# Kernel tuning notes

Measured on AMD Instinct MI355X. Metric: run time of the kernel, lower is better.

## Reference

```python
import jax, jax.numpy as jnp
import numpy as np

B, T, D = 16, 512, 256
HS, D_A, R = 512, 64, 8


def setup_inputs() -> dict:
    key = jax.random.key(0)
    ks = jax.random.split(key, 8)
    s = lambda *sh: 1.0 / np.sqrt(sh[0])
    x = jax.random.normal(ks[0], (B, T, D), dtype=jnp.float32)
    w_first = jax.random.normal(ks[1], (D, D_A), dtype=jnp.float32) * s(D)
    b_first = jnp.zeros((D_A,), dtype=jnp.float32)
    w_second = jax.random.normal(ks[2], (D_A, R), dtype=jnp.float32) * s(D_A)
    b_second = jnp.zeros((R,), dtype=jnp.float32)
    weight_iBarh = jax.random.normal(ks[3], (D, 4 * HS), dtype=jnp.float32) * s(D)
    weight_hh = jax.random.normal(ks[4], (HS, 4 * HS), dtype=jnp.float32) * s(HS)
    bias = jnp.zeros((4 * HS,), dtype=jnp.float32)
    return {"x": x, "w_first": w_first, "b_first": b_first,
            "w_second": w_second, "b_second": b_second,
            "weight_iBarh": weight_iBarh, "weight_hh": weight_hh, "bias": bias}


def _forward(x, w_first, b_first, w_second, b_second, weight_iBarh, weight_hh, bias):
    b, t, d = x.shape
    hs = weight_hh.shape[0]
    r = w_second.shape[1]
    # attention logits for every timestep: (B, T, r)
    s = jnp.tanh(x @ w_first + b_first) @ w_second + b_second
    # causal mask: query t attends to keys j <= t
    mask = jnp.tril(jnp.ones((t, t), dtype=bool))  # (t_query, j_key)
    # logits: (B, Tq, Tk, r); softmax over key axis per (t, r), masked to prefix
    logits = jnp.where(mask[None, :, :, None], s[:, None, :, :], -jnp.inf)
    attn = jax.nn.softmax(logits, axis=2).mean(axis=-1)  # (B, Tq, Tk) == mean over r
    # M_t = attention-weighted average of prefix inputs: (B, T, D)
    M = jnp.einsum('btj,bjd->btd', attn, x)
    gates_x = jnp.einsum('btd,dg->btg', M, weight_iBarh) + bias  # (B, T, 4H)

    def step(carry, gx):
        h, c = carry
        g = gx + h @ weight_hh  # (B, 4H)
        i = jax.nn.sigmoid(g[:, :hs])
        f = jax.nn.sigmoid(g[:, hs:2 * hs])
        gg = jnp.tanh(g[:, 2 * hs:3 * hs])
        o = jax.nn.sigmoid(g[:, 3 * hs:])
        c = f * c + i * gg
        h = o * jnp.tanh(c)
        return (h, c), h

    h0 = jnp.zeros((b, hs), dtype=x.dtype)
    c0 = jnp.zeros((b, hs), dtype=x.dtype)
    (h_t, c_t), hseq = jax.lax.scan(step, (h0, c0), jnp.swapaxes(gates_x, 0, 1))
    hidden_seq = jnp.swapaxes(hseq, 0, 1)  # (B, T, H)
    return hidden_seq, h_t, c_t


def reference(x, w_first, b_first, w_second, b_second, weight_iBarh, weight_hh, bias):
    return _forward(x, w_first, b_first, w_second, b_second, weight_iBarh, weight_hh, bias)
```

## Files before the change

### kernel.cpp

```cpp
#include <hip/hip_runtime.h>
#include <math.h>

#define BB 16
#define TT 512
#define DD 256
#define HS 512
#define DA 64
#define RR 8
#define G4H 2048


__global__ __launch_bounds__(256) void k1_score(
    const float* __restrict__ x, const float* __restrict__ w1,
    const float* __restrict__ b1, const float* __restrict__ w2,
    const float* __restrict__ b2, float* __restrict__ s_out) {
  const int wave = threadIdx.x >> 6;
  const int lane = threadIdx.x & 63;
  for (int i = 0; i < 4; ++i) {
    const int bt = blockIdx.x * 16 + wave * 4 + i;
    const float* xr = x + bt * DD;
    float acc = b1[lane];
    #pragma unroll 4
    for (int d = 0; d < DD; ++d)
      acc = fmaf(xr[d], w1[d * DA + lane], acc);
    const float a = tanhf(acc);
    #pragma unroll
    for (int r = 0; r < RR; ++r) {
      float v = a * w2[lane * RR + r];
      for (int off = 32; off > 0; off >>= 1) v += __shfl_xor(v, off);
      if (lane == 0) s_out[bt * RR + r] = v + b2[r];
    }
  }
}

__global__ __launch_bounds__(512) void k2_prefix(
    const float* __restrict__ s_in, float* __restrict__ e_out,
    float* __restrict__ inv_out) {
  const int b = blockIdx.x >> 3, r = blockIdx.x & 7;
  const int t = threadIdx.x;
  __shared__ float red[TT];
  __shared__ float buf[2][TT];
  const float v = s_in[(b * TT + t) * RR + r];
  red[t] = v;
  __syncthreads();
  for (int off = 256; off >= 1; off >>= 1) {
    if (t < off) red[t] = fmaxf(red[t], red[t + off]);
    __syncthreads();
  }
  const float m = red[0];
  const float e = expf(v - m);
  int p = 0;
  buf[0][t] = e;
  __syncthreads();
  for (int off = 1; off < TT; off <<= 1) {
    const float add = (t >= off) ? buf[p][t - off] : 0.f;
    buf[1 - p][t] = buf[p][t] + add;
    __syncthreads();
    p ^= 1;
  }
  const float den = buf[p][t];
  e_out[(b * TT + t) * RR + r] = e;
  inv_out[(b * TT + t) * RR + r] = 1.0f / den;
}

__global__ __launch_bounds__(64) void k3_mix(
    const float* __restrict__ x, const float* __restrict__ e_in,
    const float* __restrict__ inv_in, float* __restrict__ Mout) {
  const int b = blockIdx.x >> 2;
  const int d = (blockIdx.x & 3) * 64 + threadIdx.x;
  __shared__ __align__(16) float el[TT * RR];
  __shared__ __align__(16) float il[TT * RR];
  for (int i = threadIdx.x * 4; i < TT * RR; i += 64 * 4) {
    *(float4*)&el[i] = *(const float4*)&e_in[b * TT * RR + i];
    *(float4*)&il[i] = *(const float4*)&inv_in[b * TT * RR + i];
  }
  __syncthreads();
  float4 c0 = {0.f, 0.f, 0.f, 0.f}, c1 = {0.f, 0.f, 0.f, 0.f};
  for (int t = 0; t < TT; ++t) {
    const float xv = x[(b * TT + t) * DD + d];
    const float4 e0 = *(const float4*)&el[t * RR];
    const float4 e1 = *(const float4*)&el[t * RR + 4];
    const float4 i0 = *(const float4*)&il[t * RR];
    const float4 i1 = *(const float4*)&il[t * RR + 4];
    c0.x = fmaf(e0.x, xv, c0.x); c0.y = fmaf(e0.y, xv, c0.y);
    c0.z = fmaf(e0.z, xv, c0.z); c0.w = fmaf(e0.w, xv, c0.w);
    c1.x = fmaf(e1.x, xv, c1.x); c1.y = fmaf(e1.y, xv, c1.y);
    c1.z = fmaf(e1.z, xv, c1.z); c1.w = fmaf(e1.w, xv, c1.w);
    float msum = c0.x * i0.x + c0.y * i0.y + c0.z * i0.z + c0.w * i0.w;
    msum += c1.x * i1.x + c1.y * i1.y + c1.z * i1.z + c1.w * i1.w;
    Mout[(b * TT + t) * DD + d] = msum * 0.125f;
  }
}

__global__ __launch_bounds__(256) void k4_gemm(
    const float* __restrict__ A, const float* __restrict__ Bw,
    const float* __restrict__ bias, float* __restrict__ C) {
  const int bn = blockIdx.x & 15;
  const int bm = blockIdx.x >> 4;
  const int tid = threadIdx.x;
  const int tx = tid & 15, ty = tid >> 4;
  __shared__ __align__(16) float As[16][132];
  __shared__ __align__(16) float Bs[16][132];
  const int row0 = bm * 128, col0 = bn * 128;

  float acc[2][4][2][4];
  #pragma unroll
  for (int a = 0; a < 2; ++a)
    #pragma unroll
    for (int i = 0; i < 4; ++i)
      #pragma unroll
      for (int q = 0; q < 2; ++q)
        #pragma unroll
        for (int j = 0; j < 4; ++j) acc[a][i][q][j] = 0.f;

  const int arow = tid >> 1, akc = (tid & 1) * 8;
  const int bkr = tid >> 4, bcc = (tid & 15) * 8;

  for (int k0 = 0; k0 < 256; k0 += 16) {
    const float4 a0 = *(const float4*)&A[(row0 + arow) * 256 + k0 + akc];
    const float4 a1 = *(const float4*)&A[(row0 + arow) * 256 + k0 + akc + 4];
    const float4 b0 = *(const float4*)&Bw[(k0 + bkr) * 2048 + col0 + bcc];
    const float4 b1 = *(const float4*)&Bw[(k0 + bkr) * 2048 + col0 + bcc + 4];
    __syncthreads();
    As[akc + 0][arow] = a0.x; As[akc + 1][arow] = a0.y;
    As[akc + 2][arow] = a0.z; As[akc + 3][arow] = a0.w;
    As[akc + 4][arow] = a1.x; As[akc + 5][arow] = a1.y;
    As[akc + 6][arow] = a1.z; As[akc + 7][arow] = a1.w;
    *(float4*)&Bs[bkr][bcc] = b0;
    *(float4*)&Bs[bkr][bcc + 4] = b1;
    __syncthreads();
    #pragma unroll
    for (int kk = 0; kk < 16; ++kk) {
      float av[8], bv[8];
      *(float4*)&av[0] = *(const float4*)&As[kk][ty * 4];
      *(float4*)&av[4] = *(const float4*)&As[kk][64 + ty * 4];
      *(float4*)&bv[0] = *(const float4*)&Bs[kk][tx * 4];
      *(float4*)&bv[4] = *(const float4*)&Bs[kk][64 + tx * 4];
      #pragma unroll
      for (int a = 0; a < 2; ++a)
        #pragma unroll
        for (int i = 0; i < 4; ++i)
          #pragma unroll
          for (int q = 0; q < 2; ++q)
            #pragma unroll
            for (int j = 0; j < 4; ++j)
              acc[a][i][q][j] = fmaf(av[a * 4 + i], bv[q * 4 + j], acc[a][i][q][j]);
    }
  }
  const float4 bias0 = *(const float4*)&bias[col0 + tx * 4];
  const float4 bias1 = *(const float4*)&bias[col0 + 64 + tx * 4];
  #pragma unroll
  for (int a = 0; a < 2; ++a)
    #pragma unroll
    for (int i = 0; i < 4; ++i) {
      const int row = row0 + a * 64 + ty * 4 + i;
      float4 v0, v1;
      v0.x = acc[a][i][0][0] + bias0.x; v0.y = acc[a][i][0][1] + bias0.y;
      v0.z = acc[a][i][0][2] + bias0.z; v0.w = acc[a][i][0][3] + bias0.w;
      v1.x = acc[a][i][1][0] + bias1.x; v1.y = acc[a][i][1][1] + bias1.y;
      v1.z = acc[a][i][1][2] + bias1.z; v1.w = acc[a][i][1][3] + bias1.w;
      *(float4*)&C[row * 2048 + col0 + tx * 4] = v0;
      *(float4*)&C[row * 2048 + col0 + 64 + tx * 4] = v1;
    }
}

#define FMA4(ACC, W4, HSC)                         \
  ACC.x = fmaf((W4).x, (HSC), ACC.x);              \
  ACC.y = fmaf((W4).y, (HSC), ACC.y);              \
  ACC.z = fmaf((W4).z, (HSC), ACC.z);              \
  ACC.w = fmaf((W4).w, (HSC), ACC.w);

__device__ __forceinline__ float fast_sigmoid(float x) {
  return __builtin_amdgcn_rcpf(1.f + __expf(-x));
}
__device__ __forceinline__ float fast_tanh(float x) {
  const float xc = fmaxf(x, -30.f);
  const float e = __expf(-2.f * xc);
  return (1.f - e) * __builtin_amdgcn_rcpf(1.f + e);
}

__global__ __launch_bounds__(512, 1) void k5_lstm(
    const float* __restrict__ gates, const float* __restrict__ whh,
    float* __restrict__ out, unsigned long long* hbuf) {
  const int s   = blockIdx.x & 15;
  const int b   = blockIdx.x >> 4;
  const int tid = threadIdx.x;
  const int kq  = tid & 15;
  const int cq  = tid >> 4;
  const int j0  = s * 32;
  const int unit = j0 + cq;

  __shared__ __align__(16) float Wl[256 * 128];
  __shared__ __align__(16) float hl[2][576];

  float4 wr[32];
  for (int rnd = 0; rnd < 2; ++rnd) {
    for (int i = tid * 4; i < 256 * 128; i += 512 * 4) {
      const int k = i >> 7, c = i & 127;
      *(float4*)&Wl[i] =
          *(const float4*)&whh[(rnd * 256 + k) * G4H + (c >> 5) * HS + j0 + (c & 31)];
    }
    __syncthreads();
    if ((kq >> 3) == rnd) {
      const int kb = (kq & 7) * 32;
      #pragma unroll
      for (int kk = 0; kk < 32; ++kk) {
        const int base = (kb + kk) * 128 + cq;
        wr[kk].x = *(volatile const float*)&Wl[base];
        wr[kk].y = *(volatile const float*)&Wl[base + 32];
        wr[kk].z = *(volatile const float*)&Wl[base + 64];
        wr[kk].w = *(volatile const float*)&Wl[base + 96];
      }
    }
    __syncthreads();
  }

  float c_reg = 0.f;

  for (int t = 0; t < TT; ++t) {
    float gi = 0.f, gf = 0.f, gg = 0.f, go = 0.f;
    if (kq == 0) {
      const float* gt = gates + ((long)b * TT + t) * G4H + unit;
      gi = gt[0]; gf = gt[HS]; gg = gt[2 * HS]; go = gt[3 * HS];
    }
    const int par = t & 1;
    if (t > 0) {
      const unsigned long long* hsrc = hbuf + (((t - 1) & 1) * BB + b) * HS;
      unsigned long long pkt;
      do {
        pkt = __hip_atomic_load(&hsrc[tid], __ATOMIC_RELAXED,
                                __HIP_MEMORY_SCOPE_AGENT);
      } while ((unsigned)(pkt >> 32) < (unsigned)t);
      hl[par][(tid >> 5) * 36 + (tid & 31)] = __uint_as_float((unsigned)pkt);
    }
    __syncthreads();
    float4 acc = {0.f, 0.f, 0.f, 0.f};
    if (t > 0) {
      const float* hb = &hl[par][kq * 36];
      #pragma unroll
      for (int i = 0; i < 8; ++i) {
        const float4 h4 = *(const float4*)(hb + i * 4);
        FMA4(acc, wr[i * 4 + 0], h4.x);
        FMA4(acc, wr[i * 4 + 1], h4.y);
        FMA4(acc, wr[i * 4 + 2], h4.z);
        FMA4(acc, wr[i * 4 + 3], h4.w);
      }
    }
    #pragma unroll
    for (int off = 1; off <= 8; off <<= 1) {
      acc.x += __shfl_xor(acc.x, off); acc.y += __shfl_xor(acc.y, off);
      acc.z += __shfl_xor(acc.z, off); acc.w += __shfl_xor(acc.w, off);
    }
    if (kq == 0) {
      const float I = fast_sigmoid(acc.x + gi);
      const float F = fast_sigmoid(acc.y + gf);
      const float G = fast_tanh(acc.z + gg);
      const float O = fast_sigmoid(acc.w + go);
      c_reg = F * c_reg + I * G;
      const float h = O * fast_tanh(c_reg);
      const unsigned long long pkt =
          ((unsigned long long)(unsigned)(t + 1) << 32) |
          (unsigned long long)__float_as_uint(h);
      __hip_atomic_store(&hbuf[((t & 1) * BB + b) * HS + unit], pkt,
                         __ATOMIC_RELAXED, __HIP_MEMORY_SCOPE_AGENT);
      out[((long)b * TT + t) * HS + unit] = h;
      if (t == TT - 1) {
        out[(long)BB * TT * HS + b * HS + unit] = h;
        out[(long)BB * TT * HS + BB * HS + b * HS + unit] = c_reg;
      }
    }
  }
}

extern "C" void kernel_launch(void* const* d_in, const int* in_sizes, int n_in,
                              void* d_out, int out_size, void* d_ws,
                              size_t ws_size, hipStream_t stream) {
  const float* x    = (const float*)d_in[0];
  const float* w1   = (const float*)d_in[1];
  const float* b1   = (const float*)d_in[2];
  const float* w2   = (const float*)d_in[3];
  const float* b2   = (const float*)d_in[4];
  const float* wih  = (const float*)d_in[5];
  const float* whh  = (const float*)d_in[6];
  const float* bias = (const float*)d_in[7];
  float* out = (float*)d_out;

  float* ws = (float*)d_ws;
  float* s_buf  = ws;
  float* e_buf  = ws + 65536;
  float* i_buf  = ws + 131072;
  float* M_buf  = ws + 196608;
  float* g_buf  = ws + 2293760;
  unsigned long long* hbuf64 = (unsigned long long*)ws;

  k1_score<<<512, 256, 0, stream>>>(x, w1, b1, w2, b2, s_buf);
  k2_prefix<<<BB * RR, 512, 0, stream>>>(s_buf, e_buf, i_buf);
  k3_mix<<<64, 64, 0, stream>>>(x, e_buf, i_buf, M_buf);
  k4_gemm<<<64 * 16, 256, 0, stream>>>(M_buf, wih, bias, g_buf);
  hipMemsetAsync(hbuf64, 0, 2 * BB * HS * sizeof(unsigned long long), stream);
  k5_lstm<<<256, 512, 0, stream>>>(g_buf, whh, out, hbuf64);
}
```

Measured before the change: 1.141 ms.

## Use XCD-local sc0 polling for LSTM step handoff when batch group shares an XCD

Remaps block indices so the 16 slices of one batch element are likely placed on the same XCD, detects this at runtime via HW_REG_XCC_ID and a flag exchange, and then polls the hidden-state packets with sc0 loads that go through the XCD-local L2 instead of agent-scope atomics. Producers write with both an sc0 store and the agent-scope atomic store. If the fast poll stalls, it falls back to agent-scope polling. This is meant to cut per-timestep cross-block synchronization latency, at the cost of extra stores and reliance on undocumented cache-coherence behavior.

```diff
diff --git a/kernel.cpp b/kernel.cpp
--- a/kernel.cpp
+++ b/kernel.cpp
@@ -179,11 +179,27 @@
   return (1.f - e) * __builtin_amdgcn_rcpf(1.f + e);
 }
 
+#define HPOLL(Q) __hip_atomic_load((Q), __ATOMIC_RELAXED, __HIP_MEMORY_SCOPE_AGENT)
+
+__device__ __forceinline__ unsigned long long poll_sc0(
+    const unsigned long long* p) {
+  unsigned long long v;
+  asm volatile("global_load_dwordx2 %0, %1, off sc0\n\ts_waitcnt vmcnt(0)"
+               : "=v"(v) : "v"(p));
+  return v;
+}
+__device__ __forceinline__ void store_sc0(unsigned long long* p,
+                                          unsigned long long v) {
+  asm volatile("global_store_dwordx2 %0, %1, off sc0"
+               :: "v"(p), "v"(v) : "memory");
+}
+
 __global__ __launch_bounds__(512, 1) void k5_lstm(
     const float* __restrict__ gates, const float* __restrict__ whh,
-    float* __restrict__ out, unsigned long long* hbuf) {
-  const int s   = blockIdx.x & 15;
-  const int b   = blockIdx.x >> 4;
+    float* __restrict__ out, unsigned long long* hbuf,
+    unsigned long long* xflag) {
+  const int b   = blockIdx.x & 15;
+  const int s   = blockIdx.x >> 4;
   const int tid = threadIdx.x;
   const int kq  = tid & 15;
   const int cq  = tid >> 4;
@@ -192,6 +208,31 @@
 
   __shared__ __align__(16) float Wl[256 * 128];
   __shared__ __align__(16) float hl[2][576];
+  __shared__ int sflags[16];
+  __shared__ int s_same;
+
+  unsigned xcd;
+  asm volatile("s_getreg_b32 %0, hwreg(HW_REG_XCC_ID)" : "=s"(xcd));
+  if (tid == 0) {
+    const unsigned long long mypkt = (1ULL << 32) | (unsigned long long)xcd;
+    __hip_atomic_store(&xflag[b * 16 + s], mypkt, __ATOMIC_RELAXED,
+                       __HIP_MEMORY_SCOPE_AGENT);
+  }
+  if (tid < 16) {
+    unsigned long long v = 0; int sp = 0;
+    do {
+      v = HPOLL(&xflag[b * 16 + tid]);
+      if (++sp > 4096) break;
+    } while ((unsigned)(v >> 32) == 0u);
+    sflags[tid] =
+        ((unsigned)(v >> 32) != 0u && (unsigned)v == xcd) ? 1 : 0;
+  }
+  __syncthreads();
+  if (tid == 0) {
+    int a = 1;
+    for (int i = 0; i < 16; ++i) a &= sflags[i];
+    s_same = a;
+  }
 
   float4 wr[32];
   for (int rnd = 0; rnd < 2; ++rnd) {
@@ -214,6 +255,7 @@
     }
     __syncthreads();
   }
+  bool fast_thr = (s_same != 0);
 
   float c_reg = 0.f;
 
@@ -225,12 +267,24 @@
     }
     const int par = t & 1;
     if (t > 0) {
-      const unsigned long long* hsrc = hbuf + (((t - 1) & 1) * BB + b) * HS;
+      const unsigned long long* hsrc =
+          hbuf + (((t - 1) & 1) * BB + b) * HS + tid;
+      const unsigned tt = (unsigned)t;
       unsigned long long pkt;
-      do {
-        pkt = __hip_atomic_load(&hsrc[tid], __ATOMIC_RELAXED,
-                                __HIP_MEMORY_SCOPE_AGENT);
-      } while ((unsigned)(pkt >> 32) < (unsigned)t);
+      if (fast_thr) {
+        int spins = 0; bool ok = false;
+        for (;;) {
+          pkt = poll_sc0(hsrc);
+          if ((unsigned)(pkt >> 32) >= tt) { ok = true; break; }
+          if (++spins == 8) break;
+        }
+        if (!ok) {
+          if (t >= 8) fast_thr = false;
+          do { pkt = HPOLL(hsrc); } while ((unsigned)(pkt >> 32) < tt);
+        }
+      } else {
+        do { pkt = HPOLL(hsrc); } while ((unsigned)(pkt >> 32) < tt);
+      }
       hl[par][(tid >> 5) * 36 + (tid & 31)] = __uint_as_float((unsigned)pkt);
     }
     __syncthreads();
@@ -261,8 +315,10 @@
       const unsigned long long pkt =
           ((unsigned long long)(unsigned)(t + 1) << 32) |
           (unsigned long long)__float_as_uint(h);
-      __hip_atomic_store(&hbuf[((t & 1) * BB + b) * HS + unit], pkt,
-                         __ATOMIC_RELAXED, __HIP_MEMORY_SCOPE_AGENT);
+      unsigned long long* dst = &hbuf[((t & 1) * BB + b) * HS + unit];
+      store_sc0(dst, pkt);
+      __hip_atomic_store(dst, pkt, __ATOMIC_RELAXED,
+                         __HIP_MEMORY_SCOPE_AGENT);
       out[((long)b * TT + t) * HS + unit] = h;
       if (t == TT - 1) {
         out[(long)BB * TT * HS + b * HS + unit] = h;
@@ -292,11 +348,13 @@
   float* M_buf  = ws + 196608;
   float* g_buf  = ws + 2293760;
   unsigned long long* hbuf64 = (unsigned long long*)ws;
+  unsigned long long* xflag  = hbuf64 + 2 * BB * HS;
 
   k1_score<<<512, 256, 0, stream>>>(x, w1, b1, w2, b2, s_buf);
   k2_prefix<<<BB * RR, 512, 0, stream>>>(s_buf, e_buf, i_buf);
   k3_mix<<<64, 64, 0, stream>>>(x, e_buf, i_buf, M_buf);
   k4_gemm<<<64 * 16, 256, 0, stream>>>(M_buf, wih, bias, g_buf);
-  hipMemsetAsync(hbuf64, 0, 2 * BB * HS * sizeof(unsigned long long), stream);
-  k5_lstm<<<256, 512, 0, stream>>>(g_buf, whh, out, hbuf64);
-}
+  hipMemsetAsync(hbuf64, 0,
+                 (2 * BB * HS + 256) * sizeof(unsigned long long), stream);
+  k5_lstm<<<256, 512, 0, stream>>>(g_buf, whh, out, hbuf64, xflag);
+}
```

Result: slower. 2.533 ms (+122.1%).

## Fuse input-projection GEMM into persistent LSTM kernel using LDS-resident W_ih slice

Applied to the files above, without the earlier changes.

Removes the separate gates GEMM and its gates buffer. Each LSTM block now keeps its slice of W_ih in shared memory and computes M_t·W_ih for its units inside the recurrence. The next timestep's M row is prefetched into a double-buffered LDS slot, and the input projection is placed before the h-poll so it can overlap the wait on other blocks. The trade is extra FMAs and LDS reads on the serial critical path of every step, in place of one bulk parallel GEMM and a global gates read.

```diff
diff --git a/kernel.cpp b/kernel.cpp
--- a/kernel.cpp
+++ b/kernel.cpp
@@ -92,78 +92,6 @@
   }
 }
 
-__global__ __launch_bounds__(256) void k4_gemm(
-    const float* __restrict__ A, const float* __restrict__ Bw,
-    const float* __restrict__ bias, float* __restrict__ C) {
-  const int bn = blockIdx.x & 15;
-  const int bm = blockIdx.x >> 4;
-  const int tid = threadIdx.x;
-  const int tx = tid & 15, ty = tid >> 4;
-  __shared__ __align__(16) float As[16][132];
-  __shared__ __align__(16) float Bs[16][132];
-  const int row0 = bm * 128, col0 = bn * 128;
-
-  float acc[2][4][2][4];
-  #pragma unroll
-  for (int a = 0; a < 2; ++a)
-    #pragma unroll
-    for (int i = 0; i < 4; ++i)
-      #pragma unroll
-      for (int q = 0; q < 2; ++q)
-        #pragma unroll
-        for (int j = 0; j < 4; ++j) acc[a][i][q][j] = 0.f;
-
-  const int arow = tid >> 1, akc = (tid & 1) * 8;
-  const int bkr = tid >> 4, bcc = (tid & 15) * 8;
-
-  for (int k0 = 0; k0 < 256; k0 += 16) {
-    const float4 a0 = *(const float4*)&A[(row0 + arow) * 256 + k0 + akc];
-    const float4 a1 = *(const float4*)&A[(row0 + arow) * 256 + k0 + akc + 4];
-    const float4 b0 = *(const float4*)&Bw[(k0 + bkr) * 2048 + col0 + bcc];
-    const float4 b1 = *(const float4*)&Bw[(k0 + bkr) * 2048 + col0 + bcc + 4];
-    __syncthreads();
-    As[akc + 0][arow] = a0.x; As[akc + 1][arow] = a0.y;
-    As[akc + 2][arow] = a0.z; As[akc + 3][arow] = a0.w;
-    As[akc + 4][arow] = a1.x; As[akc + 5][arow] = a1.y;
-    As[akc + 6][arow] = a1.z; As[akc + 7][arow] = a1.w;
-    *(float4*)&Bs[bkr][bcc] = b0;
-    *(float4*)&Bs[bkr][bcc + 4] = b1;
-    __syncthreads();
-    #pragma unroll
-    for (int kk = 0; kk < 16; ++kk) {
-      float av[8], bv[8];
-      *(float4*)&av[0] = *(const float4*)&As[kk][ty * 4];
-      *(float4*)&av[4] = *(const float4*)&As[kk][64 + ty * 4];
-      *(float4*)&bv[0] = *(const float4*)&Bs[kk][tx * 4];
-      *(float4*)&bv[4] = *(const float4*)&Bs[kk][64 + tx * 4];
-      #pragma unroll
-      for (int a = 0; a < 2; ++a)
-        #pragma unroll
-        for (int i = 0; i < 4; ++i)
-          #pragma unroll
-          for (int q = 0; q < 2; ++q)
-            #pragma unroll
-            for (int j = 0; j < 4; ++j)
-              acc[a][i][q][j] = fmaf(av[a * 4 + i], bv[q * 4 + j], acc[a][i][q][j]);
-    }
-  }
-  const float4 bias0 = *(const float4*)&bias[col0 + tx * 4];
-  const float4 bias1 = *(const float4*)&bias[col0 + 64 + tx * 4];
-  #pragma unroll
-  for (int a = 0; a < 2; ++a)
-    #pragma unroll
-    for (int i = 0; i < 4; ++i) {
-      const int row = row0 + a * 64 + ty * 4 + i;
-      float4 v0, v1;
-      v0.x = acc[a][i][0][0] + bias0.x; v0.y = acc[a][i][0][1] + bias0.y;
-      v0.z = acc[a][i][0][2] + bias0.z; v0.w = acc[a][i][0][3] + bias0.w;
-      v1.x = acc[a][i][1][0] + bias1.x; v1.y = acc[a][i][1][1] + bias1.y;
-      v1.z = acc[a][i][1][2] + bias1.z; v1.w = acc[a][i][1][3] + bias1.w;
-      *(float4*)&C[row * 2048 + col0 + tx * 4] = v0;
-      *(float4*)&C[row * 2048 + col0 + 64 + tx * 4] = v1;
-    }
-}
-
 #define FMA4(ACC, W4, HSC)                         \
   ACC.x = fmaf((W4).x, (HSC), ACC.x);              \
   ACC.y = fmaf((W4).y, (HSC), ACC.y);              \
@@ -179,8 +107,11 @@
   return (1.f - e) * __builtin_amdgcn_rcpf(1.f + e);
 }
 
+#define HPOLL(Q) __hip_atomic_load((Q), __ATOMIC_RELAXED, __HIP_MEMORY_SCOPE_AGENT)
+
 __global__ __launch_bounds__(512, 1) void k5_lstm(
-    const float* __restrict__ gates, const float* __restrict__ whh,
+    const float* __restrict__ Mrow, const float* __restrict__ whh,
+    const float* __restrict__ wih, const float* __restrict__ bias,
     float* __restrict__ out, unsigned long long* hbuf) {
   const int s   = blockIdx.x & 15;
   const int b   = blockIdx.x >> 4;
@@ -190,8 +121,9 @@
   const int j0  = s * 32;
   const int unit = j0 + cq;
 
-  __shared__ __align__(16) float Wl[256 * 128];
+  __shared__ __align__(16) float Wl[16 * 2052];
   __shared__ __align__(16) float hl[2][576];
+  __shared__ __align__(16) float M_lds[2][320];
 
   float4 wr[32];
   for (int rnd = 0; rnd < 2; ++rnd) {
@@ -215,26 +147,57 @@
     __syncthreads();
   }
 
+  for (int m = tid * 4; m < 32768; m += 2048) {
+    const int g_kq = m >> 11, g_i = (m >> 7) & 15, g_cq = (m >> 2) & 31;
+    const int row = g_kq * 16 + g_i;
+    float4 w4;
+    w4.x = wih[row * G4H + 0 * HS + j0 + g_cq];
+    w4.y = wih[row * G4H + 1 * HS + j0 + g_cq];
+    w4.z = wih[row * G4H + 2 * HS + j0 + g_cq];
+    w4.w = wih[row * G4H + 3 * HS + j0 + g_cq];
+    *(float4*)&Wl[g_kq * 2052 + g_i * 128 + g_cq * 4] = w4;
+  }
+  if (tid < 64)
+    *(float4*)&M_lds[0][(tid >> 2) * 20 + (tid & 3) * 4] =
+        *(const float4*)&Mrow[(long)b * TT * DD + tid * 4];
+  float bi = 0.f, bf = 0.f, bg = 0.f, bo = 0.f;
+  if (kq == 0) {
+    bi = bias[unit];          bf = bias[HS + unit];
+    bg = bias[2 * HS + unit]; bo = bias[3 * HS + unit];
+  }
+  __syncthreads();
+
   float c_reg = 0.f;
 
   for (int t = 0; t < TT; ++t) {
-    float gi = 0.f, gf = 0.f, gg = 0.f, go = 0.f;
-    if (kq == 0) {
-      const float* gt = gates + ((long)b * TT + t) * G4H + unit;
-      gi = gt[0]; gf = gt[HS]; gg = gt[2 * HS]; go = gt[3 * HS];
-    }
     const int par = t & 1;
+    float4 mnext = {0.f, 0.f, 0.f, 0.f};
+    if (tid < 64) {
+      const int tn = (t + 1 < TT) ? t + 1 : t;
+      mnext = *(const float4*)&Mrow[((long)b * TT + tn) * DD + tid * 4];
+    }
+    float4 acc = {0.f, 0.f, 0.f, 0.f};
+    {
+      const float* Lp = &Wl[kq * 2052 + cq * 4];
+      const float* mp = &M_lds[par][kq * 20];
+      #pragma unroll
+      for (int i = 0; i < 16; ++i) {
+        const float4 w4 = *(const float4*)(Lp + i * 128);
+        const float mv = mp[i];
+        FMA4(acc, w4, mv);
+      }
+    }
+    asm volatile("" : "+v"(acc.x), "+v"(acc.y), "+v"(acc.z), "+v"(acc.w));
     if (t > 0) {
-      const unsigned long long* hsrc = hbuf + (((t - 1) & 1) * BB + b) * HS;
+      const unsigned long long* hsrc =
+          hbuf + (((t - 1) & 1) * BB + b) * HS + tid;
       unsigned long long pkt;
-      do {
-        pkt = __hip_atomic_load(&hsrc[tid], __ATOMIC_RELAXED,
-                                __HIP_MEMORY_SCOPE_AGENT);
-      } while ((unsigned)(pkt >> 32) < (unsigned)t);
+      do { pkt = HPOLL(hsrc); } while ((unsigned)(pkt >> 32) < (unsigned)t);
       hl[par][(tid >> 5) * 36 + (tid & 31)] = __uint_as_float((unsigned)pkt);
     }
-    __syncthreads();
-    float4 acc = {0.f, 0.f, 0.f, 0.f};
+    if (tid < 64)
+      *(float4*)&M_lds[par ^ 1][(tid >> 2) * 20 + (tid & 3) * 4] = mnext;
+    __syncthreads();
     if (t > 0) {
       const float* hb = &hl[par][kq * 36];
       #pragma unroll
@@ -252,10 +215,10 @@
       acc.z += __shfl_xor(acc.z, off); acc.w += __shfl_xor(acc.w, off);
     }
     if (kq == 0) {
-      const float I = fast_sigmoid(acc.x + gi);
-      const float F = fast_sigmoid(acc.y + gf);
-      const float G = fast_tanh(acc.z + gg);
-      const float O = fast_sigmoid(acc.w + go);
+      const float I = fast_sigmoid(acc.x + bi);
+      const float F = fast_sigmoid(acc.y + bf);
+      const float G = fast_tanh(acc.z + bg);
+      const float O = fast_sigmoid(acc.w + bo);
       c_reg = F * c_reg + I * G;
       const float h = O * fast_tanh(c_reg);
       const unsigned long long pkt =
@@ -290,13 +253,11 @@
   float* e_buf  = ws + 65536;
   float* i_buf  = ws + 131072;
   float* M_buf  = ws + 196608;
-  float* g_buf  = ws + 2293760;
   unsigned long long* hbuf64 = (unsigned long long*)ws;
 
   k1_score<<<512, 256, 0, stream>>>(x, w1, b1, w2, b2, s_buf);
   k2_prefix<<<BB * RR, 512, 0, stream>>>(s_buf, e_buf, i_buf);
   k3_mix<<<64, 64, 0, stream>>>(x, e_buf, i_buf, M_buf);
-  k4_gemm<<<64 * 16, 256, 0, stream>>>(M_buf, wih, bias, g_buf);
   hipMemsetAsync(hbuf64, 0, 2 * BB * HS * sizeof(unsigned long long), stream);
-  k5_lstm<<<256, 512, 0, stream>>>(g_buf, whh, out, hbuf64);
-}
+  k5_lstm<<<256, 512, 0, stream>>>(M_buf, whh, wih, bias, out, hbuf64);
+}
```

After: 1.061 ms. -7.0%, faster.
